# Performance work log

Hardware: AMD Instinct MI355X
Metric: run time of the kernel (lower is better)

The kernel has to match this reference:

```python
import jax, jax.numpy as jnp
import numpy as np

N_SPIKES = 1_000_000
N_SAMPLES = 64          # waveform length, hard-coded as 64 in the original
K_SEG = 257             # cluster ids 0..256; 0 = CLID_UNMATCHED
FIRST_MATCH_FACTOR = 1.5
FIRST_MATCH_MAX_DIST = 4.0
CLID_UNMATCHED = 0
BIG = 1e30              # finite stand-in for +inf (keeps grads clean)


def setup_inputs() -> dict:
    key = jax.random.key(0)
    k1, k2 = jax.random.split(key)
    spikes = jax.random.normal(k1, (N_SPIKES, N_SAMPLES), dtype=jnp.float32)
    sort_idx = jax.random.randint(k2, (N_SPIKES,), 0, K_SEG, dtype=jnp.int32)
    match_idx = jnp.zeros((N_SPIKES,), dtype=jnp.bool_)
    return {"spikes": spikes, "sort_idx": sort_idx, "match_idx": match_idx}


def reference(spikes, sort_idx, match_idx):
    # --- get_means: per-cluster mean waveform and std (ddof=0), vectorized via segment_sum ---
    ones = jnp.ones((spikes.shape[0],), dtype=spikes.dtype)
    counts = jax.ops.segment_sum(ones, sort_idx, num_segments=K_SEG)          # (K,)
    sums = jax.ops.segment_sum(spikes, sort_idx, num_segments=K_SEG)          # (K, 64)
    sumsq = jax.ops.segment_sum(spikes * spikes, sort_idx, num_segments=K_SEG)
    safe_cnt = jnp.maximum(counts, 1.0)[:, None]
    means = sums / safe_cnt                                                   # (K, 64)
    var = jnp.maximum(sumsq / safe_cnt - means * means, 0.0)                  # biased var per feature
    stds = jnp.sqrt(var.sum(axis=1))                                          # (K,)

    cluster_ids = jnp.arange(K_SEG)
    valid = (cluster_ids != CLID_UNMATCHED) & (counts > 0)

    # --- exclude_variable_clusters: drop clusters with std > 3 * median(std) ---
    median_std = jnp.nanmedian(jnp.where(valid, stds, jnp.nan))
    valid = valid & (stds <= 3.0 * median_std)

    # --- euclidean distances spike->template via ||s||^2 - 2 s.t + ||t||^2 (same math, no (M,K,64) blowup) ---
    sn = jnp.sum(spikes * spikes, axis=1)                                      # (M,)
    tn = jnp.sum(means * means, axis=1)                                        # (K,)
    d2 = sn[:, None] - 2.0 * (spikes @ means.T) + tn[None, :]                  # (M, K)
    dists = jnp.sqrt(jnp.maximum(d2, 0.0))

    # threshold mask: dist > factor*std  OR  invalid cluster  ->  effectively inf
    masked = (dists > FIRST_MATCH_FACTOR * stds[None, :]) | (~valid[None, :])
    dists = jnp.where(masked, BIG, dists)

    min_vals = jnp.min(dists, axis=1)                                          # (M,)
    minimizers = jnp.argmin(dists, axis=1).astype(sort_idx.dtype)              # segment index == cluster id

    # absolute max-distance cutoff (also kills all-masked rows since BIG >> 4*64)
    minimizers = jnp.where(min_vals >= FIRST_MATCH_MAX_DIST * N_SAMPLES,
                           CLID_UNMATCHED, minimizers)

    unmatched = sort_idx == CLID_UNMATCHED
    new_sort_idx = jnp.where(unmatched, minimizers, sort_idx)
    new_match_idx = jnp.where(unmatched, minimizers != CLID_UNMATCHED, match_idx)
    return new_sort_idx, new_match_idx, min_vals
```

## Files before the change

kernel.cpp:

```cpp
#include <hip/hip_runtime.h>

#define NCLUST 256
#define NFEAT  64
#define NBLK_A 256
#define BIGF   1e30f

#define SUM_SCALE  1073741824.0
#define SSQ_SCALE  16777216.0
#define INV_SUM_SCALE (1.0 / 1073741824.0)
#define INV_SSQ_SCALE (1.0 / 16777216.0)

typedef __attribute__((ext_vector_type(8))) short  short8v;
typedef __attribute__((ext_vector_type(4))) float  float4v;
typedef unsigned long long u64;

__device__ __align__(16) u64      g_psum[(size_t)NCLUST * NBLK_A * NFEAT];
__device__ __align__(16) u64      g_pssq[(size_t)NCLUST * NBLK_A * 8];
__device__ unsigned g_pcnt[NCLUST * NBLK_A * 8];
__device__ float  g_cnt[NCLUST];
__device__ __align__(16) double g_means64[NCLUST * NFEAT];
__device__ __align__(16) double g_means64T[NFEAT * NCLUST];
__device__ __align__(16) float  g_means32[NCLUST * NFEAT];
__device__ __align__(16) unsigned short g_tmplbf[NCLUST * NFEAT];
__device__ double g_tn64[NCLUST];
__device__ double g_std64[NCLUST];
__device__ float  g_std32[NCLUST];
__device__ float2 g_ktab[NCLUST];
__device__ int    g_valid[NCLUST];
__device__ int    g_list[1000000];
__device__ int    g_nlist;

static __device__ __forceinline__ unsigned short f2bf(float x) {
    union { float f; unsigned u; } v; v.f = x;
    unsigned r = v.u + 0x7fffu + ((v.u >> 16) & 1u);
    return (unsigned short)(r >> 16);
}

__global__ void kzero() { if (threadIdx.x == 0) g_nlist = 0; }

__global__ __launch_bounds__(1024, 4) void kstats(const float* __restrict__ spikes,
                                                  const int* __restrict__ sidx, int n) {
    __shared__ u64      lsum[NCLUST * NFEAT];
    __shared__ u64      lssq[NCLUST * 8];
    __shared__ unsigned lcnt[NCLUST * 8];
    for (int idx = threadIdx.x; idx < NCLUST * NFEAT; idx += 1024) lsum[idx] = 0ull;
    for (int idx = threadIdx.x; idx < NCLUST * 8; idx += 1024) { lssq[idx] = 0ull; lcnt[idx] = 0u; }
    __syncthreads();

    const int lane = threadIdx.x & 63;
    const int wave = threadIdx.x >> 6;
    const int per  = (n + gridDim.x - 1) / gridDim.x;
    const int s0   = blockIdx.x * per;
    const int s1   = min(n, s0 + per);

    for (int ib = s0 + wave * 8; ib < s1; ib += 16 * 8) {
        float v[8]; int c[8];
        #pragma unroll
        for (int j = 0; j < 8; ++j) {
            int i  = ib + j;
            int rc = (i < s1) ? i : (s1 - 1);
            v[j] = spikes[(size_t)rc * NFEAT + lane];
            c[j] = (i < s1) ? sidx[i] : 0;
        }
        #pragma unroll
        for (int j = 0; j < 8; ++j) {
            int cj = c[j];
            if (cj != 0) {
                double vd = (double)v[j];
                long long sv = llrint(vd * SUM_SCALE);
                long long qv = llrint(vd * vd * SSQ_SCALE);
                atomicAdd(&lsum[(cj - 1) * NFEAT + lane], (u64)sv);
                atomicAdd(&lssq[(cj - 1) * 8 + (lane & 7)], (u64)qv);
                if (lane == 0) atomicAdd(&lcnt[(cj - 1) * 8 + (wave & 7)], 1u);
            }
        }
    }
    __syncthreads();

    const int b = blockIdx.x;
    for (int idx = threadIdx.x; idx < NCLUST * NFEAT; idx += 1024) {
        int c = idx >> 6, f = idx & 63;
        g_psum[((size_t)c * NBLK_A + b) * NFEAT + f] = lsum[idx];
    }
    for (int idx = threadIdx.x; idx < NCLUST * 8; idx += 1024) {
        int c = idx >> 3, k = idx & 7;
        g_pssq[((size_t)c * NBLK_A + b) * 8 + k] = lssq[idx];
        g_pcnt[(c * NBLK_A + b) * 8 + k]         = lcnt[idx];
    }
}

__global__ __launch_bounds__(256) void kfinal() {
    const int c = blockIdx.x;
    __shared__ u64 redS[4][NFEAT];
    __shared__ double smean[NFEAT];
    __shared__ double sh_cnt, sh_ssq;
    const int f = threadIdx.x & 63, j = threadIdx.x >> 6;

    u64 acc = 0ull;
    for (int b = j; b < NBLK_A; b += 4)
        acc += g_psum[((size_t)c * NBLK_A + b) * NFEAT + f];
    redS[j][f] = acc;

    if (threadIdx.x < 64) {
        u64 sq = 0ull; unsigned cn = 0u;
        for (int e = threadIdx.x; e < NBLK_A * 8; e += 64) {
            sq += g_pssq[(size_t)c * NBLK_A * 8 + e];
            cn += g_pcnt[c * NBLK_A * 8 + e];
        }
        #pragma unroll
        for (int o = 32; o; o >>= 1) {
            sq += __shfl_xor(sq, o);
            cn += __shfl_xor(cn, o);
        }
        if (threadIdx.x == 0) {
            sh_cnt = (double)cn;
            sh_ssq = (double)(long long)sq * INV_SSQ_SCALE;
        }
    }
    __syncthreads();

    if (threadIdx.x < NFEAT) {
        long long tot = (long long)(redS[0][f] + redS[1][f] + redS[2][f] + redS[3][f]);
        double cnt = sh_cnt;
        double mean = (cnt > 0.0) ? ((double)tot * INV_SUM_SCALE) / cnt : 0.0;
        g_means64[c * NFEAT + f]  = mean;
        g_means64T[f * NCLUST + c] = mean;
        g_means32[c * NFEAT + f]  = (float)mean;
        smean[f] = mean;
    }
    __syncthreads();
    if (threadIdx.x == 0) {
        double tn = 0.0;
        for (int q = 0; q < NFEAT; ++q) tn += smean[q] * smean[q];
        double cnt = sh_cnt;
        double var = (cnt > 0.0) ? sh_ssq / cnt - tn : 0.0;
        if (var < 0.0) var = 0.0;
        double sd = sqrt(var);
        g_tn64[c] = tn; g_std64[c] = sd; g_std32[c] = (float)sd;
        g_cnt[c] = (float)cnt;
    }
}

__global__ __launch_bounds__(256) void kmedian() {
    __shared__ float svals[NCLUST];
    __shared__ int   svalid[NCLUST];
    __shared__ float mred[2];
    int t = threadIdx.x;
    if (t == 0) { mred[0] = 0.f; mred[1] = 0.f; }
    float cnt = g_cnt[t];
    int v0 = (cnt > 0.f) ? 1 : 0;
    float sd = g_std32[t];
    svals[t] = sd; svalid[t] = v0;
    __syncthreads();

    int m = 0, rank = 0;
    for (int jj = 0; jj < NCLUST; ++jj) {
        if (svalid[jj]) {
            ++m;
            float sj = svals[jj];
            if (sj < sd || (sj == sd && jj < t)) ++rank;
        }
    }
    if (v0) {
        if (rank == (m - 1) / 2) mred[0] = sd;
        if (rank == m / 2)       mred[1] = sd;
    }
    __syncthreads();
    float med = 0.5f * (mred[0] + mred[1]);

    int valid = v0 && (sd <= 3.0f * med);
    double sd64 = g_std64[t];
    float thr2 = valid ? (float)((1.5 * sd64) * (1.5 * sd64)) : -1.0f;
    g_valid[t] = valid;
    g_ktab[t]  = make_float2((float)g_tn64[t], thr2);

    for (int q = threadIdx.x; q < NCLUST * 8; q += 256) {
        int c = q >> 3, g = q & 7;
        float4 u0 = *(const float4*)&g_means32[c * NFEAT + g * 8];
        float4 u1 = *(const float4*)&g_means32[c * NFEAT + g * 8 + 4];
        short8v h;
        h[0] = (short)f2bf(u0.x); h[1] = (short)f2bf(u0.y);
        h[2] = (short)f2bf(u0.z); h[3] = (short)f2bf(u0.w);
        h[4] = (short)f2bf(u1.x); h[5] = (short)f2bf(u1.y);
        h[6] = (short)f2bf(u1.z); h[7] = (short)f2bf(u1.w);
        unsigned byteoff = (unsigned)c * 128u + (((unsigned)g * 16u) ^ (((unsigned)c & 7u) << 4));
        *(short8v*)((char*)g_tmplbf + byteoff) = h;
    }
}

__global__ __launch_bounds__(256) void kmatch(const float* __restrict__ spikes,
                                              const int* __restrict__ sidx,
                                              const unsigned char* __restrict__ midx,
                                              float* __restrict__ out, int n) {
    __shared__ __align__(16) unsigned short tml[NCLUST * NFEAT];
    __shared__ float2 ktab_sh[NCLUST];

    for (int idx = threadIdx.x * 8; idx < NCLUST * NFEAT; idx += 256 * 8)
        *(short8v*)&tml[idx] = *(const short8v*)&g_tmplbf[idx];
    if (threadIdx.x < NCLUST) ktab_sh[threadIdx.x] = g_ktab[threadIdx.x];
    __syncthreads();

    const int lane = threadIdx.x & 63, wave = threadIdx.x >> 6;
    const int row  = lane & 15, grp = lane >> 4;
    const int i0w  = blockIdx.x * 256 + wave * 64;

    #pragma unroll 1
    for (int sb = 0; sb < 4; ++sb) {
        const int i0 = i0w + sb * 16;

        int ri = i0 + row;
        int rc = (ri < n) ? ri : (n - 1);
        const float* sp = spikes + (size_t)rc * NFEAT + grp * 8;
        float4 a0 = *(const float4*)(sp);
        float4 a1 = *(const float4*)(sp + 4);
        float4 a2 = *(const float4*)(sp + 32);
        float4 a3 = *(const float4*)(sp + 36);
        short8v af0, af1;
        af0[0] = (short)f2bf(a0.x); af0[1] = (short)f2bf(a0.y);
        af0[2] = (short)f2bf(a0.z); af0[3] = (short)f2bf(a0.w);
        af0[4] = (short)f2bf(a1.x); af0[5] = (short)f2bf(a1.y);
        af0[6] = (short)f2bf(a1.z); af0[7] = (short)f2bf(a1.w);
        af1[0] = (short)f2bf(a2.x); af1[1] = (short)f2bf(a2.y);
        af1[2] = (short)f2bf(a2.z); af1[3] = (short)f2bf(a2.w);
        af1[4] = (short)f2bf(a3.x); af1[5] = (short)f2bf(a3.y);
        af1[6] = (short)f2bf(a3.z); af1[7] = (short)f2bf(a3.w);

        float pss = a0.x*a0.x + a0.y*a0.y + a0.z*a0.z + a0.w*a0.w
                  + a1.x*a1.x + a1.y*a1.y + a1.z*a1.z + a1.w*a1.w
                  + a2.x*a2.x + a2.y*a2.y + a2.z*a2.z + a2.w*a2.w
                  + a3.x*a3.x + a3.y*a3.y + a3.z*a3.z + a3.w*a3.w;
        pss += __shfl_xor(pss, 16);
        pss += __shfl_xor(pss, 32);

        float snr[4];
        #pragma unroll
        for (int r = 0; r < 4; ++r) snr[r] = __shfl(pss, grp * 4 + r);

        float d2min[4] = {3.4e38f, 3.4e38f, 3.4e38f, 3.4e38f};

        #pragma unroll 2
        for (int nt = 0; nt < 16; ++nt) {
            int c = nt * 16 + row;
            unsigned co = (unsigned)c * 128u;
            unsigned sw = (((unsigned)c & 7u) << 4);
            short8v b0 = *(short8v*)((char*)tml + (co + (((unsigned)grp * 16u) ^ sw)));
            short8v b1 = *(short8v*)((char*)tml + (co + ((((unsigned)grp + 4u) * 16u) ^ sw)));
            float4v acc = {0.f, 0.f, 0.f, 0.f};
            acc = __builtin_amdgcn_mfma_f32_16x16x32_bf16(af0, b0, acc, 0, 0, 0);
            acc = __builtin_amdgcn_mfma_f32_16x16x32_bf16(af1, b1, acc, 0, 0, 0);
            float2 kt = ktab_sh[c];
            #pragma unroll
            for (int r = 0; r < 4; ++r) {
                float d2 = (snr[r] - 2.0f * acc[r]) + kt.x;
                if (!(d2 > kt.y)) d2min[r] = fminf(d2min[r], d2);
            }
        }

        #pragma unroll
        for (int o = 1; o < 16; o <<= 1) {
            #pragma unroll
            for (int r = 0; r < 4; ++r) d2min[r] = fminf(d2min[r], __shfl_xor(d2min[r], o));
        }
        if (row == 0) {
            #pragma unroll
            for (int r = 0; r < 4; ++r) {
                int i = i0 + grp * 4 + r;
                if (i < n) {
                    float dm = d2min[r];
                    out[2 * (size_t)n + i] = (dm > 1e37f) ? BIGF : sqrtf(fmaxf(dm, 0.f));
                }
            }
        }
    }

    int i = blockIdx.x * 256 + threadIdx.x;
    if (i < n) {
        int si = sidx[i];
        out[i]             = (float)si;
        out[(size_t)n + i] = midx[i] ? 1.0f : 0.0f;
        if (si == 0) {
            int p = atomicAdd(&g_nlist, 1);
            if (p < 1000000) g_list[p] = i;
        }
    }
}

__global__ __launch_bounds__(256) void kprecise(const float* __restrict__ spikes,
                                                float* __restrict__ out, int n) {
    const int lane  = threadIdx.x & 63;
    const int gwave = (blockIdx.x * 256 + threadIdx.x) >> 6;
    const int nwave = (gridDim.x * 256) >> 6;
    const int nt    = g_nlist;

    double tn[4], thr[4]; int vld[4];
    #pragma unroll
    for (int q = 0; q < 4; ++q) {
        int c = q * 64 + lane;
        tn[q]  = g_tn64[c];
        thr[q] = 1.5 * g_std64[c];
        vld[q] = g_valid[c];
    }

    for (int t = gwave; t < nt; t += nwave) {
        const int i = g_list[t];
        const double sf = (double)spikes[(size_t)i * NFEAT + lane];

        double sn = sf * sf;
        #pragma unroll
        for (int o = 32; o; o >>= 1) sn += __shfl_xor(sn, o);

        double d0 = 0.0, d1 = 0.0, d2a = 0.0, d3 = 0.0;
        #pragma unroll 16
        for (int f = 0; f < NFEAT; ++f) {
            double b = __shfl(sf, f);
            const double* mrow = &g_means64T[(size_t)f * NCLUST + lane];
            d0 = fma(b, mrow[0],   d0);
            d1 = fma(b, mrow[64],  d1);
            d2a = fma(b, mrow[128], d2a);
            d3 = fma(b, mrow[192], d3);
        }
        double dot[4] = {d0, d1, d2a, d3};

        double dmin = 1e30; int best = 0;
        #pragma unroll
        for (int q = 0; q < 4; ++q) {
            if (!vld[q]) continue;
            double d2 = (sn - 2.0 * dot[q]) + tn[q];
            double dist = sqrt(fmax(d2, 0.0));
            if (dist > thr[q]) continue;
            if (dist < dmin) { dmin = dist; best = q * 64 + lane + 1; }
        }

        #pragma unroll
        for (int o = 32; o; o >>= 1) {
            double od = __shfl_xor(dmin, o);
            int    ob = __shfl_xor(best, o);
            if (od < dmin || (od == dmin && ob < best)) { dmin = od; best = ob; }
        }

        if (dmin >= 256.0) best = 0;

        if (lane == 0) {
            out[i]                 = (float)best;
            out[(size_t)n + i]     = (best != 0) ? 1.0f : 0.0f;
            out[2 * (size_t)n + i] = (float)dmin;
        }
    }
}

extern "C" void kernel_launch(void* const* d_in, const int* in_sizes, int n_in,
                              void* d_out, int out_size, void* d_ws, size_t ws_size,
                              hipStream_t stream) {
    const float*         spikes = (const float*)d_in[0];
    const int*           sidx   = (const int*)d_in[1];
    const unsigned char* midx   = (const unsigned char*)d_in[2];
    float*               out    = (float*)d_out;
    const int n = in_sizes[1];

    kzero<<<1, 64, 0, stream>>>();
    kstats<<<NBLK_A, 1024, 0, stream>>>(spikes, sidx, n);
    kfinal<<<NCLUST, 256, 0, stream>>>();
    kmedian<<<1, 256, 0, stream>>>();
    int nblk = (n + 255) / 256;
    kmatch<<<nblk, 256, 0, stream>>>(spikes, sidx, midx, out, n);
    kprecise<<<1024, 256, 0, stream>>>(spikes, out, n);
}
```

Baseline: 250.4 us.

## Use 32-bit fixed-point LDS atomics in stats pass and fold small kernels

Replaces the 64-bit shared-memory atomics with 32-bit integer atomics at smaller fixed-point scales, computed in float rather than double. The sum of squares is now kept per feature instead of in 8 folded bins. Each lane loads a float2, so one wave covers two spikes per step. The bf16 template packing moves into kfinal, and the g_nlist reset moves into kmedian, which drops the kzero launch and the g_means32 buffer. This cuts double-precision conversion work and 64-bit atomic cost in the stats pass, in exchange for lower fixed-point resolution and a risk of 32-bit overflow in per-block partial sums.

```diff
diff --git a/kernel.cpp b/kernel.cpp
--- a/kernel.cpp
+++ b/kernel.cpp
@@ -5,22 +5,21 @@
 #define NBLK_A 256
 #define BIGF   1e30f
 
-#define SUM_SCALE  1073741824.0
-#define SSQ_SCALE  16777216.0
-#define INV_SUM_SCALE (1.0 / 1073741824.0)
-#define INV_SSQ_SCALE (1.0 / 16777216.0)
+#define SUMSC  16777216.0f
+#define SSQSC  2097152.0f
+#define INV_SUMSC (1.0 / 16777216.0)
+#define INV_SSQSC (1.0 / 2097152.0)
 
 typedef __attribute__((ext_vector_type(8))) short  short8v;
 typedef __attribute__((ext_vector_type(4))) float  float4v;
 typedef unsigned long long u64;
 
-__device__ __align__(16) u64      g_psum[(size_t)NCLUST * NBLK_A * NFEAT];
-__device__ __align__(16) u64      g_pssq[(size_t)NCLUST * NBLK_A * 8];
+__device__ __align__(16) unsigned g_psum[(size_t)NCLUST * NBLK_A * NFEAT];
+__device__ __align__(16) unsigned g_pssq[(size_t)NCLUST * NBLK_A * NFEAT];
 __device__ unsigned g_pcnt[NCLUST * NBLK_A * 8];
 __device__ float  g_cnt[NCLUST];
 __device__ __align__(16) double g_means64[NCLUST * NFEAT];
 __device__ __align__(16) double g_means64T[NFEAT * NCLUST];
-__device__ __align__(16) float  g_means32[NCLUST * NFEAT];
 __device__ __align__(16) unsigned short g_tmplbf[NCLUST * NFEAT];
 __device__ double g_tn64[NCLUST];
 __device__ double g_std64[NCLUST];
@@ -36,42 +35,42 @@
     return (unsigned short)(r >> 16);
 }
 
-__global__ void kzero() { if (threadIdx.x == 0) g_nlist = 0; }
-
 __global__ __launch_bounds__(1024, 4) void kstats(const float* __restrict__ spikes,
                                                   const int* __restrict__ sidx, int n) {
-    __shared__ u64      lsum[NCLUST * NFEAT];
-    __shared__ u64      lssq[NCLUST * 8];
+    __shared__ unsigned lsum[NCLUST * NFEAT];
+    __shared__ unsigned lssq[NCLUST * NFEAT];
     __shared__ unsigned lcnt[NCLUST * 8];
-    for (int idx = threadIdx.x; idx < NCLUST * NFEAT; idx += 1024) lsum[idx] = 0ull;
-    for (int idx = threadIdx.x; idx < NCLUST * 8; idx += 1024) { lssq[idx] = 0ull; lcnt[idx] = 0u; }
+    for (int idx = threadIdx.x; idx < NCLUST * NFEAT; idx += 1024) { lsum[idx] = 0u; lssq[idx] = 0u; }
+    for (int idx = threadIdx.x; idx < NCLUST * 8; idx += 1024) lcnt[idx] = 0u;
     __syncthreads();
 
     const int lane = threadIdx.x & 63;
     const int wave = threadIdx.x >> 6;
+    const int half = lane >> 5;
+    const int m    = lane & 31;
     const int per  = (n + gridDim.x - 1) / gridDim.x;
     const int s0   = blockIdx.x * per;
     const int s1   = min(n, s0 + per);
 
-    for (int ib = s0 + wave * 8; ib < s1; ib += 16 * 8) {
-        float v[8]; int c[8];
-        #pragma unroll
-        for (int j = 0; j < 8; ++j) {
-            int i  = ib + j;
+    for (int ib = s0 + wave * 16; ib < s1; ib += 16 * 16) {
+        float2 v[8]; int cc[8];
+        #pragma unroll
+        for (int p = 0; p < 8; ++p) {
+            int i  = ib + p * 2 + half;
             int rc = (i < s1) ? i : (s1 - 1);
-            v[j] = spikes[(size_t)rc * NFEAT + lane];
-            c[j] = (i < s1) ? sidx[i] : 0;
-        }
-        #pragma unroll
-        for (int j = 0; j < 8; ++j) {
-            int cj = c[j];
-            if (cj != 0) {
-                double vd = (double)v[j];
-                long long sv = llrint(vd * SUM_SCALE);
-                long long qv = llrint(vd * vd * SSQ_SCALE);
-                atomicAdd(&lsum[(cj - 1) * NFEAT + lane], (u64)sv);
-                atomicAdd(&lssq[(cj - 1) * 8 + (lane & 7)], (u64)qv);
-                if (lane == 0) atomicAdd(&lcnt[(cj - 1) * 8 + (wave & 7)], 1u);
+            v[p]  = *(const float2*)(spikes + (size_t)rc * NFEAT + m * 2);
+            cc[p] = (i < s1) ? sidx[i] : 0;
+        }
+        #pragma unroll
+        for (int p = 0; p < 8; ++p) {
+            int c = cc[p];
+            if (c != 0) {
+                int base = (c - 1) * NFEAT + m * 2;
+                atomicAdd(&lsum[base],     (unsigned)__float2int_rn(v[p].x * SUMSC));
+                atomicAdd(&lsum[base + 1], (unsigned)__float2int_rn(v[p].y * SUMSC));
+                atomicAdd(&lssq[base],     (unsigned)__float2int_rn(v[p].x * v[p].x * SSQSC));
+                atomicAdd(&lssq[base + 1], (unsigned)__float2int_rn(v[p].y * v[p].y * SSQSC));
+                if (m == 0) atomicAdd(&lcnt[(c - 1) * 8 + (wave & 7)], 1u);
             }
         }
     }
@@ -81,59 +80,59 @@
     for (int idx = threadIdx.x; idx < NCLUST * NFEAT; idx += 1024) {
         int c = idx >> 6, f = idx & 63;
         g_psum[((size_t)c * NBLK_A + b) * NFEAT + f] = lsum[idx];
+        g_pssq[((size_t)c * NBLK_A + b) * NFEAT + f] = lssq[idx];
     }
     for (int idx = threadIdx.x; idx < NCLUST * 8; idx += 1024) {
         int c = idx >> 3, k = idx & 7;
-        g_pssq[((size_t)c * NBLK_A + b) * 8 + k] = lssq[idx];
-        g_pcnt[(c * NBLK_A + b) * 8 + k]         = lcnt[idx];
+        g_pcnt[(c * NBLK_A + b) * 8 + k] = lcnt[idx];
     }
 }
 
 __global__ __launch_bounds__(256) void kfinal() {
     const int c = blockIdx.x;
-    __shared__ u64 redS[4][NFEAT];
+    __shared__ long long red [4][NFEAT];
+    __shared__ long long redq[4][NFEAT];
     __shared__ double smean[NFEAT];
-    __shared__ double sh_cnt, sh_ssq;
+    __shared__ double sh_cnt;
     const int f = threadIdx.x & 63, j = threadIdx.x >> 6;
 
-    u64 acc = 0ull;
-    for (int b = j; b < NBLK_A; b += 4)
-        acc += g_psum[((size_t)c * NBLK_A + b) * NFEAT + f];
-    redS[j][f] = acc;
+    long long acc = 0, accq = 0;
+    for (int b = j; b < NBLK_A; b += 4) {
+        acc  += (int)g_psum[((size_t)c * NBLK_A + b) * NFEAT + f];
+        accq += (int)g_pssq[((size_t)c * NBLK_A + b) * NFEAT + f];
+    }
+    red[j][f] = acc; redq[j][f] = accq;
 
     if (threadIdx.x < 64) {
-        u64 sq = 0ull; unsigned cn = 0u;
-        for (int e = threadIdx.x; e < NBLK_A * 8; e += 64) {
-            sq += g_pssq[(size_t)c * NBLK_A * 8 + e];
+        unsigned cn = 0u;
+        for (int e = threadIdx.x; e < NBLK_A * 8; e += 64)
             cn += g_pcnt[c * NBLK_A * 8 + e];
-        }
-        #pragma unroll
-        for (int o = 32; o; o >>= 1) {
-            sq += __shfl_xor(sq, o);
-            cn += __shfl_xor(cn, o);
-        }
-        if (threadIdx.x == 0) {
-            sh_cnt = (double)cn;
-            sh_ssq = (double)(long long)sq * INV_SSQ_SCALE;
-        }
+        #pragma unroll
+        for (int o = 32; o; o >>= 1) cn += __shfl_xor(cn, o);
+        if (threadIdx.x == 0) sh_cnt = (double)cn;
     }
     __syncthreads();
 
     if (threadIdx.x < NFEAT) {
-        long long tot = (long long)(redS[0][f] + redS[1][f] + redS[2][f] + redS[3][f]);
+        long long tot = ((red[0][f] + red[1][f]) + red[2][f]) + red[3][f];
         double cnt = sh_cnt;
-        double mean = (cnt > 0.0) ? ((double)tot * INV_SUM_SCALE) / cnt : 0.0;
-        g_means64[c * NFEAT + f]  = mean;
+        double mean = (cnt > 0.0) ? ((double)tot * INV_SUMSC) / cnt : 0.0;
+        g_means64[c * NFEAT + f]   = mean;
         g_means64T[f * NCLUST + c] = mean;
-        g_means32[c * NFEAT + f]  = (float)mean;
         smean[f] = mean;
+        redq[0][f] = ((redq[0][f] + redq[1][f]) + redq[2][f]) + redq[3][f];
+        unsigned short hb = f2bf((float)mean);
+        unsigned g = (unsigned)(f >> 3);
+        unsigned byteoff = (unsigned)c * 128u
+                         + (((g * 16u) ^ (((unsigned)c & 7u) << 4)) + (unsigned)(f & 7) * 2u);
+        *(unsigned short*)((char*)g_tmplbf + byteoff) = hb;
     }
     __syncthreads();
     if (threadIdx.x == 0) {
-        double tn = 0.0;
-        for (int q = 0; q < NFEAT; ++q) tn += smean[q] * smean[q];
+        double tn = 0.0; long long qs = 0;
+        for (int q = 0; q < NFEAT; ++q) { tn += smean[q] * smean[q]; qs += redq[0][q]; }
         double cnt = sh_cnt;
-        double var = (cnt > 0.0) ? sh_ssq / cnt - tn : 0.0;
+        double var = (cnt > 0.0) ? ((double)qs * INV_SSQSC) / cnt - tn : 0.0;
         if (var < 0.0) var = 0.0;
         double sd = sqrt(var);
         g_tn64[c] = tn; g_std64[c] = sd; g_std32[c] = (float)sd;
@@ -146,7 +145,7 @@
     __shared__ int   svalid[NCLUST];
     __shared__ float mred[2];
     int t = threadIdx.x;
-    if (t == 0) { mred[0] = 0.f; mred[1] = 0.f; }
+    if (t == 0) { mred[0] = 0.f; mred[1] = 0.f; g_nlist = 0; }
     float cnt = g_cnt[t];
     int v0 = (cnt > 0.f) ? 1 : 0;
     float sd = g_std32[t];
@@ -173,19 +172,6 @@
     float thr2 = valid ? (float)((1.5 * sd64) * (1.5 * sd64)) : -1.0f;
     g_valid[t] = valid;
     g_ktab[t]  = make_float2((float)g_tn64[t], thr2);
-
-    for (int q = threadIdx.x; q < NCLUST * 8; q += 256) {
-        int c = q >> 3, g = q & 7;
-        float4 u0 = *(const float4*)&g_means32[c * NFEAT + g * 8];
-        float4 u1 = *(const float4*)&g_means32[c * NFEAT + g * 8 + 4];
-        short8v h;
-        h[0] = (short)f2bf(u0.x); h[1] = (short)f2bf(u0.y);
-        h[2] = (short)f2bf(u0.z); h[3] = (short)f2bf(u0.w);
-        h[4] = (short)f2bf(u1.x); h[5] = (short)f2bf(u1.y);
-        h[6] = (short)f2bf(u1.z); h[7] = (short)f2bf(u1.w);
-        unsigned byteoff = (unsigned)c * 128u + (((unsigned)g * 16u) ^ (((unsigned)c & 7u) << 4));
-        *(short8v*)((char*)g_tmplbf + byteoff) = h;
-    }
 }
 
 __global__ __launch_bounds__(256) void kmatch(const float* __restrict__ spikes,
@@ -357,7 +343,6 @@
     float*               out    = (float*)d_out;
     const int n = in_sizes[1];
 
-    kzero<<<1, 64, 0, stream>>>();
     kstats<<<NBLK_A, 1024, 0, stream>>>(spikes, sidx, n);
     kfinal<<<NCLUST, 256, 0, stream>>>();
     kmedian<<<1, 256, 0, stream>>>();
```

Measured after the change: 210.5 us. 15.9% less time.
